# Performance work log

Measured on AMD Instinct MI355X. Metric: run time of the kernel, lower is better.

## Reference

```python
import jax, jax.numpy as jnp
import numpy as np

H = 32  # hidden_size fixed by the module
I = 1   # input_size

def setup_inputs() -> dict:
    key = jax.random.key(0)
    ks = jax.random.split(key, 8)
    B, T = 8192, 512
    s = 0.1
    return {
        "x": jax.random.normal(ks[0], (B, T, I), dtype=jnp.float32),
        "W_ih": jax.random.normal(ks[1], (4 * H, I), dtype=jnp.float32) * s,
        "W_hh": jax.random.normal(ks[2], (4 * H, H), dtype=jnp.float32) * s,
        "b_ih": jax.random.normal(ks[3], (4 * H,), dtype=jnp.float32) * s,
        "b_hh": jax.random.normal(ks[4], (4 * H,), dtype=jnp.float32) * s,
        "W_lin": jax.random.normal(ks[5], (1, H), dtype=jnp.float32) * s,
        "b_lin": jax.random.normal(ks[6], (1,), dtype=jnp.float32) * s,
    }

def _lstm_last_hidden(x, W_ih, W_hh, b_ih, b_hh):
    B = x.shape[0]
    # Precompute input contribution to all gates: [B, T, 4H] -> scan over T.
    xg = jnp.einsum('bti,gi->btg', x, W_ih) + b_ih + b_hh
    xg = jnp.swapaxes(xg, 0, 1)  # [T, B, 4H]

    def step(carry, xg_t):
        h, c = carry
        gates = xg_t + h @ W_hh.T  # [B, 4H]
        i, f, g, o = jnp.split(gates, 4, axis=-1)  # PyTorch gate order i,f,g,o
        i = jax.nn.sigmoid(i)
        f = jax.nn.sigmoid(f)
        g = jnp.tanh(g)
        o = jax.nn.sigmoid(o)
        c = f * c + i * g
        h = o * jnp.tanh(c)
        return (h, c), None

    h0 = jnp.zeros((B, H), dtype=x.dtype)
    c0 = jnp.zeros((B, H), dtype=x.dtype)
    (h_last, _), _ = jax.lax.scan(step, (h0, c0), xg)
    return h_last  # [B, H] == out[:, -1, :]

def reference(x, W_ih, W_hh, b_ih, b_hh, W_lin, b_lin):
    h_last = _lstm_last_hidden(x, W_ih, W_hh, b_ih, b_hh)
    return h_last @ W_lin.T + b_lin  # [B, 1]
```

## Files before the change

kernel.cpp:

```cpp
#include <hip/hip_runtime.h>


#define L2E 1.4426950408889634f

typedef _Float16 f16x8 __attribute__((ext_vector_type(8)));
typedef float    f32x4 __attribute__((ext_vector_type(4)));

__global__ __launch_bounds__(512, 4) void lstm_ctile(
    const float* __restrict__ x,
    const float* __restrict__ W_ih,
    const float* __restrict__ W_hh,
    const float* __restrict__ b_ih,
    const float* __restrict__ b_hh,
    const float* __restrict__ W_lin,
    const float* __restrict__ b_lin,
    float* __restrict__ out)
{
    __shared__ float xs[512 * 17];
    __shared__ __align__(16) unsigned int hb[2][16 * 20];
    __shared__ float ps[128];

    const int tid  = threadIdx.x;
    const int wv   = tid >> 6;
    const int hf   = wv >> 2;
    const int rs   = wv & 3;
    const int lane = tid & 63;
    const int col  = lane & 15;
    const int quad = lane >> 4;
    const int base = blockIdx.x * 16;

    {
        const float4* xg = (const float4*)(x + (size_t)base * 512);
        #pragma unroll
        for (int it = 0; it < 4; ++it) {
            int idx = it * 512 + tid;
            float4 v = xg[idx];
            int b  = idx >> 7;
            int t0 = (idx & 127) * 4;
            xs[(t0 + 0) * 17 + b] = v.x;
            xs[(t0 + 1) * 17 + b] = v.y;
            xs[(t0 + 2) * 17 + b] = v.z;
            xs[(t0 + 3) * 17 + b] = v.w;
        }
    }

    f16x8 wA;
    {
        const int Tm = col & 3;
        const float s = (Tm == 2) ? (2.0f * L2E) : L2E;
        const int grow = 32 * Tm + 16 * hf + 4 * (col >> 2) + rs;
        #pragma unroll
        for (int j = 0; j < 8; ++j)
            wA[j] = (_Float16)(W_hh[grow * 32 + quad * 8 + j] * s);
    }
    const int jj = 16 * hf + 4 * quad + rs;
    float wih1[4], bia1[4];
    #pragma unroll
    for (int r = 0; r < 4; ++r) {
        const float s = (r == 2) ? (2.0f * L2E) : L2E;
        const int g = 32 * r + jj;
        wih1[r] = W_ih[g] * s;
        bia1[r] = (b_ih[g] + b_hh[g]) * s;
    }
    const float wl = W_lin[jj];

    __syncthreads();

    float c0 = 0.0f, h0 = 0.0f;
    f16x8 bfrag = {};
    f32x4 cq;
    {
        float xt = xs[col];
        #pragma unroll
        for (int r = 0; r < 4; ++r)
            cq[r] = fmaf(xt, wih1[r], bia1[r]);
    }

    #pragma unroll 2
    for (int t = 0; t < 512; ++t) {
        unsigned int* buf = hb[t & 1];

        f32x4 acc = __builtin_amdgcn_mfma_f32_16x16x32_f16(wA, bfrag, cq, 0, 0, 0);

        float xt1 = xs[((t + 1) & 511) * 17 + col];

        float ei = __builtin_amdgcn_exp2f(-acc[0]);
        float ef = __builtin_amdgcn_exp2f(-acc[1]);
        float eg = __builtin_amdgcn_exp2f(-acc[2]);
        float eo = __builtin_amdgcn_exp2f(-acc[3]);
        float aI = 1.0f + ei, aF = 1.0f + ef, aG = 1.0f + eg, aO = 1.0f + eo;
        float gN = 1.0f - eg;
        float tIG = aI * aG;
        float num = fmaf(c0, tIG, gN * aF);
        float rcD = __builtin_amdgcn_rcpf(aF * tIG);
        c0 = num * rcD;
        float ec = __builtin_amdgcn_exp2f(c0 * (-2.0f * L2E));
        float aC = 1.0f + ec, cN = 1.0f - ec;
        float rcH = __builtin_amdgcn_rcpf(aO * aC);
        h0 = cN * rcH;

        ((short*)buf)[col * 40 + jj] =
            (short)__builtin_bit_cast(unsigned short, (_Float16)h0);

        #pragma unroll
        for (int r = 0; r < 4; ++r)
            cq[r] = fmaf(xt1, wih1[r], bia1[r]);

        __syncthreads();
        uint4 bv = *(const uint4*)&buf[col * 20 + quad * 4];
        bfrag = __builtin_bit_cast(f16x8, bv);
    }

    float v = h0 * wl;
    v += __shfl_xor(v, 16);
    v += __shfl_xor(v, 32);
    if (lane < 16) ps[wv * 16 + col] = v;
    __syncthreads();
    if (tid < 16) {
        float s = b_lin[0];
        #pragma unroll
        for (int w = 0; w < 8; ++w) s += ps[w * 16 + tid];
        out[base + tid] = s;
    }
}

extern "C" void kernel_launch(void* const* d_in, const int* in_sizes, int n_in,
                              void* d_out, int out_size, void* d_ws, size_t ws_size,
                              hipStream_t stream) {
    const float* x     = (const float*)d_in[0];
    const float* W_ih  = (const float*)d_in[1];
    const float* W_hh  = (const float*)d_in[2];
    const float* b_ih  = (const float*)d_in[3];
    const float* b_hh  = (const float*)d_in[4];
    const float* W_lin = (const float*)d_in[5];
    const float* b_lin = (const float*)d_in[6];
    float* out = (float*)d_out;

    const int B = in_sizes[0] / 512;
    dim3 grid(B / 16), block(512);
    lstm_ctile<<<grid, block, 0, stream>>>(x, W_ih, W_hh, b_ih, b_hh, W_lin, b_lin, out);
}
```

Before: 237.6 us.

## Halve block size so each wave computes two hidden units per step

The 16-sample LSTM tile now runs on 4 waves instead of 8. Each lane issues two MFMAs per timestep and evaluates the gate nonlinearities for two hidden units, then writes both h values to shared memory as one packed fp16 pair. The goal is to cut the per-step barrier cost among fewer waves and to raise ILP, since the two independent gate chains can interleave. The trade-off is a longer serial chain per wave on each step and higher register use.

```diff
diff --git a/kernel.cpp b/kernel.cpp
--- a/kernel.cpp
+++ b/kernel.cpp
@@ -6,7 +6,7 @@
 typedef _Float16 f16x8 __attribute__((ext_vector_type(8)));
 typedef float    f32x4 __attribute__((ext_vector_type(4)));
 
-__global__ __launch_bounds__(512, 4) void lstm_ctile(
+__global__ __launch_bounds__(256, 4) void lstm_ct4(
     const float* __restrict__ x,
     const float* __restrict__ W_ih,
     const float* __restrict__ W_hh,
@@ -18,12 +18,10 @@
 {
     __shared__ float xs[512 * 17];
     __shared__ __align__(16) unsigned int hb[2][16 * 20];
-    __shared__ float ps[128];
+    __shared__ float ps[64];
 
     const int tid  = threadIdx.x;
     const int wv   = tid >> 6;
-    const int hf   = wv >> 2;
-    const int rs   = wv & 3;
     const int lane = tid & 63;
     const int col  = lane & 15;
     const int quad = lane >> 4;
@@ -32,8 +30,8 @@
     {
         const float4* xg = (const float4*)(x + (size_t)base * 512);
         #pragma unroll
-        for (int it = 0; it < 4; ++it) {
-            int idx = it * 512 + tid;
+        for (int it = 0; it < 8; ++it) {
+            int idx = it * 256 + tid;
             float4 v = xg[idx];
             int b  = idx >> 7;
             int t0 = (idx & 127) * 4;
@@ -44,84 +42,98 @@
         }
     }
 
-    f16x8 wA;
-    {
-        const int Tm = col & 3;
-        const float s = (Tm == 2) ? (2.0f * L2E) : L2E;
-        const int grow = 32 * Tm + 16 * hf + 4 * (col >> 2) + rs;
+    f16x8 wA[2];
+    #pragma unroll
+    for (int tau = 0; tau < 2; ++tau) {
+        const int rt = col & 3;
+        const float s = (rt == 2) ? (2.0f * L2E) : L2E;
+        const int grow = 32 * rt + 8 * wv + 2 * (col >> 2) + tau;
         #pragma unroll
         for (int j = 0; j < 8; ++j)
-            wA[j] = (_Float16)(W_hh[grow * 32 + quad * 8 + j] * s);
+            wA[tau][j] = (_Float16)(W_hh[grow * 32 + quad * 8 + j] * s);
     }
-    const int jj = 16 * hf + 4 * quad + rs;
-    float wih1[4], bia1[4];
+    const int j0 = 8 * wv + 2 * quad;
+    float wih[2][4], bia[2][4];
     #pragma unroll
-    for (int r = 0; r < 4; ++r) {
-        const float s = (r == 2) ? (2.0f * L2E) : L2E;
-        const int g = 32 * r + jj;
-        wih1[r] = W_ih[g] * s;
-        bia1[r] = (b_ih[g] + b_hh[g]) * s;
-    }
-    const float wl = W_lin[jj];
+    for (int tau = 0; tau < 2; ++tau)
+        #pragma unroll
+        for (int r = 0; r < 4; ++r) {
+            const float s = (r == 2) ? (2.0f * L2E) : L2E;
+            const int g = 32 * r + j0 + tau;
+            wih[tau][r] = W_ih[g] * s;
+            bia[tau][r] = (b_ih[g] + b_hh[g]) * s;
+        }
+    const float wl0 = W_lin[j0], wl1 = W_lin[j0 + 1];
 
     __syncthreads();
 
-    float c0 = 0.0f, h0 = 0.0f;
+    float c0 = 0.0f, c1 = 0.0f, h0 = 0.0f, h1 = 0.0f;
     f16x8 bfrag = {};
-    f32x4 cq;
+    f32x4 cq[2];
     {
         float xt = xs[col];
         #pragma unroll
-        for (int r = 0; r < 4; ++r)
-            cq[r] = fmaf(xt, wih1[r], bia1[r]);
+        for (int tau = 0; tau < 2; ++tau)
+            #pragma unroll
+            for (int r = 0; r < 4; ++r)
+                cq[tau][r] = fmaf(xt, wih[tau][r], bia[tau][r]);
     }
 
-    #pragma unroll 2
+    const int wr = col * 20 + 4 * wv + quad;
+
+    #pragma unroll 4
     for (int t = 0; t < 512; ++t) {
         unsigned int* buf = hb[t & 1];
 
-        f32x4 acc = __builtin_amdgcn_mfma_f32_16x16x32_f16(wA, bfrag, cq, 0, 0, 0);
+        f32x4 a0 = __builtin_amdgcn_mfma_f32_16x16x32_f16(wA[0], bfrag, cq[0], 0, 0, 0);
+        f32x4 a1 = __builtin_amdgcn_mfma_f32_16x16x32_f16(wA[1], bfrag, cq[1], 0, 0, 0);
 
         float xt1 = xs[((t + 1) & 511) * 17 + col];
 
-        float ei = __builtin_amdgcn_exp2f(-acc[0]);
-        float ef = __builtin_amdgcn_exp2f(-acc[1]);
-        float eg = __builtin_amdgcn_exp2f(-acc[2]);
-        float eo = __builtin_amdgcn_exp2f(-acc[3]);
-        float aI = 1.0f + ei, aF = 1.0f + ef, aG = 1.0f + eg, aO = 1.0f + eo;
-        float gN = 1.0f - eg;
-        float tIG = aI * aG;
-        float num = fmaf(c0, tIG, gN * aF);
-        float rcD = __builtin_amdgcn_rcpf(aF * tIG);
-        c0 = num * rcD;
-        float ec = __builtin_amdgcn_exp2f(c0 * (-2.0f * L2E));
-        float aC = 1.0f + ec, cN = 1.0f - ec;
-        float rcH = __builtin_amdgcn_rcpf(aO * aC);
-        h0 = cN * rcH;
+        float ei0 = __builtin_amdgcn_exp2f(-a0[0]);
+        float ef0 = __builtin_amdgcn_exp2f(-a0[1]);
+        float eg0 = __builtin_amdgcn_exp2f(-a0[2]);
+        float eo0 = __builtin_amdgcn_exp2f(-a0[3]);
+        float ei1 = __builtin_amdgcn_exp2f(-a1[0]);
+        float ef1 = __builtin_amdgcn_exp2f(-a1[1]);
+        float eg1 = __builtin_amdgcn_exp2f(-a1[2]);
+        float eo1 = __builtin_amdgcn_exp2f(-a1[3]);
+        float aI0 = 1.0f + ei0, aF0 = 1.0f + ef0, aG0 = 1.0f + eg0, aO0 = 1.0f + eo0;
+        float aI1 = 1.0f + ei1, aF1 = 1.0f + ef1, aG1 = 1.0f + eg1, aO1 = 1.0f + eo1;
+        float tIG0 = aI0 * aG0, tIG1 = aI1 * aG1;
+        float num0 = fmaf(c0, tIG0, (1.0f - eg0) * aF0);
+        float num1 = fmaf(c1, tIG1, (1.0f - eg1) * aF1);
+        float rcD0 = __builtin_amdgcn_rcpf(aF0 * tIG0);
+        float rcD1 = __builtin_amdgcn_rcpf(aF1 * tIG1);
+        c0 = num0 * rcD0;
+        c1 = num1 * rcD1;
+        float ec0 = __builtin_amdgcn_exp2f(c0 * (-2.0f * L2E));
+        float ec1 = __builtin_amdgcn_exp2f(c1 * (-2.0f * L2E));
+        float rcH0 = __builtin_amdgcn_rcpf(aO0 * (1.0f + ec0));
+        float rcH1 = __builtin_amdgcn_rcpf(aO1 * (1.0f + ec1));
+        h0 = (1.0f - ec0) * rcH0;
+        h1 = (1.0f - ec1) * rcH1;
 
-        ((short*)buf)[col * 40 + jj] =
-            (short)__builtin_bit_cast(unsigned short, (_Float16)h0);
+        buf[wr] = __builtin_bit_cast(unsigned int, __builtin_amdgcn_cvt_pkrtz(h0, h1));
 
         #pragma unroll
-        for (int r = 0; r < 4; ++r)
-            cq[r] = fmaf(xt1, wih1[r], bia1[r]);
+        for (int tau = 0; tau < 2; ++tau)
+            #pragma unroll
+            for (int r = 0; r < 4; ++r)
+                cq[tau][r] = fmaf(xt1, wih[tau][r], bia[tau][r]);
 
         __syncthreads();
         uint4 bv = *(const uint4*)&buf[col * 20 + quad * 4];
         bfrag = __builtin_bit_cast(f16x8, bv);
     }
 
-    float v = h0 * wl;
+    float v = fmaf(h0, wl0, h1 * wl1);
     v += __shfl_xor(v, 16);
     v += __shfl_xor(v, 32);
     if (lane < 16) ps[wv * 16 + col] = v;
     __syncthreads();
-    if (tid < 16) {
-        float s = b_lin[0];
-        #pragma unroll
-        for (int w = 0; w < 8; ++w) s += ps[w * 16 + tid];
-        out[base + tid] = s;
-    }
+    if (tid < 16)
+        out[base + tid] = b_lin[0] + ps[tid] + ps[16 + tid] + ps[32 + tid] + ps[48 + tid];
 }
 
 extern "C" void kernel_launch(void* const* d_in, const int* in_sizes, int n_in,
@@ -137,6 +149,6 @@
     float* out = (float*)d_out;
 
     const int B = in_sizes[0] / 512;
-    dim3 grid(B / 16), block(512);
-    lstm_ctile<<<grid, block, 0, stream>>>(x, W_ih, W_hh, b_ih, b_hh, W_lin, b_lin, out);
+    dim3 grid(B / 16), block(256);
+    lstm_ct4<<<grid, block, 0, stream>>>(x, W_ih, W_hh, b_ih, b_hh, W_lin, b_lin, out);
 }
```

Result: faster. 222.0 us (-6.6%).
